# Performance work log

Measured on AMD Instinct MI355X. Metric: run time of the kernel, lower is better.

Reference implementation:

```python
import jax, jax.numpy as jnp
import numpy as np

V, D, H, L, S, B, FF, MAXLEN = 50257, 768, 12, 12, 1024, 4, 3072, 1024
HD = D // H
EPS = 1e-5


def layernorm(x, w, b):
    m = jnp.mean(x, axis=-1, keepdims=True)
    v = jnp.mean(jnp.square(x - m), axis=-1, keepdims=True)
    return (x - m) * jax.lax.rsqrt(v + EPS) * w + b


def setup_inputs() -> dict:
    key = jax.random.key(0)
    ks = jax.random.split(key, 8)
    std = 0.02
    return {
        "tokens": jax.random.randint(ks[0], (B, S), 0, V, dtype=jnp.int32),
        "wte": std * jax.random.normal(ks[1], (V, D), jnp.float32),
        "wpe": std * jax.random.normal(ks[2], (1, MAXLEN, D), jnp.float32),
        "ln1_w": jnp.ones((L, D), jnp.float32),
        "ln1_b": jnp.zeros((L, D), jnp.float32),
        "ln2_w": jnp.ones((L, D), jnp.float32),
        "ln2_b": jnp.zeros((L, D), jnp.float32),
        "W_exp": std * jax.random.normal(ks[3], (L, D, 3 * D), jnp.float32),
        "b_exp": jnp.zeros((L, 3 * D), jnp.float32),
        "W_o": std * jax.random.normal(ks[4], (L, D, D), jnp.float32),
        "b_o": jnp.zeros((L, D), jnp.float32),
        "W_ff1": std * jax.random.normal(ks[5], (L, D, FF), jnp.float32),
        "b_ff1": jnp.zeros((L, FF), jnp.float32),
        "W_ff2": std * jax.random.normal(ks[6], (L, FF, D), jnp.float32),
        "b_ff2": jnp.zeros((L, D), jnp.float32),
    }


def reference(tokens, wte, wpe, ln1_w, ln1_b, ln2_w, ln2_b,
              W_exp, b_exp, W_o, b_o, W_ff1, b_ff1, W_ff2, b_ff2):
    Bc, Sc = tokens.shape
    x = wte[tokens] + wpe[:, :Sc, :]                      # [B,S,D]
    mask = jnp.tril(jnp.ones((Sc, Sc), bool))             # causal (past=None)
    scale = 1.0 / jnp.sqrt(jnp.float32(HD))
    presents = []
    for l in range(L):
        h = layernorm(x, ln1_w[l], ln1_b[l])
        qkv = h @ W_exp[l] + b_exp[l]                     # [B,S,3D]
        q, k, v = jnp.split(qkv, 3, axis=-1)
        q = q.reshape(Bc, Sc, H, HD)
        k = k.reshape(Bc, Sc, H, HD)
        v = v.reshape(Bc, Sc, H, HD)
        presents.append(jnp.stack([k, v]))                # [2,B,S,H,HD]
        score = jnp.einsum('bqhd,bkhd->bhqk', q, k)
        score = jnp.where(mask, score, jnp.float32(-1e20))
        attn = jax.nn.softmax(score * scale, axis=-1)     # mask applied BEFORE scaling, as in source
        a = jnp.einsum('bhqk,bkhd->bqhd', attn, v).reshape(Bc, Sc, D)
        a = a @ W_o[l] + b_o[l]
        add = layernorm(a + x, ln2_w[l], ln2_b[l])        # LN2 on residual sum (GPT2-variant in source)
        ff = jax.nn.gelu(add @ W_ff1[l] + b_ff1[l], approximate=False)
        ff = ff @ W_ff2[l] + b_ff2[l]
        x = ff + add
    return x, jnp.stack(presents)                         # [L,2,B,S,H,HD]
```

## Files before the change

kernel.cpp:

```cpp
#include <hip/hip_runtime.h>
#include <hip/hip_bf16.h>
#include <math.h>

#define Bc 4
#define Sc 1024
#define Dc 768
#define Hc 12
#define Lc 12
#define FFc 3072
#define Mtot (Bc*Sc)

typedef __bf16 bf16x8 __attribute__((ext_vector_type(8)));
typedef float f32x4 __attribute__((ext_vector_type(4)));

__device__ __forceinline__ void gload_lds16(const void* g, void* l) {
    __builtin_amdgcn_global_load_lds((const __attribute__((address_space(1))) void*)g,
                                     (__attribute__((address_space(3))) void*)l, 16, 0, 0);
}

__global__ __launch_bounds__(256) void embed_kernel(const int* __restrict__ tokens,
                                                    const float* __restrict__ wte,
                                                    const float* __restrict__ wpe,
                                                    float* __restrict__ x) {
    int row = blockIdx.x;
    int s = row & (Sc - 1);
    int tok = tokens[row];
    const float* wt = wte + (size_t)tok * Dc;
    const float* wp = wpe + (size_t)s * Dc;
    float* xr = x + (size_t)row * Dc;
#pragma unroll
    for (int k = 0; k < 3; ++k) {
        int d = threadIdx.x + k * 256;
        xr[d] = wt[d] + wp[d];
    }
}

__global__ __launch_bounds__(256) void transpose_kernel(const float* __restrict__ W,
                                                        __bf16* __restrict__ WT,
                                                        int K, int N) {
    __shared__ float t[32][33];
    int l = blockIdx.z;
    const float* Wl = W + (size_t)l * K * N;
    __bf16* WTl = WT + (size_t)l * K * N;
    int n0 = blockIdx.x * 32, k0 = blockIdx.y * 32;
    int tx = threadIdx.x & 31, ty = threadIdx.x >> 5;
#pragma unroll
    for (int i = 0; i < 4; ++i)
        t[ty + 8 * i][tx] = Wl[(size_t)(k0 + ty + 8 * i) * N + n0 + tx];
    __syncthreads();
#pragma unroll
    for (int i = 0; i < 4; ++i)
        WTl[(size_t)(n0 + ty + 8 * i) * K + k0 + tx] = (__bf16)t[tx][ty + 8 * i];
}

template <bool DUAL>
__global__ __launch_bounds__(256) void ln_kernel(const float* __restrict__ x,
                                                 const float* __restrict__ lw,
                                                 const float* __restrict__ lb,
                                                 __bf16* __restrict__ outb,
                                                 float* __restrict__ outf) {
    int row = blockIdx.x;
    const float* xr = x + (size_t)row * Dc;
    int t = threadIdx.x;
    float v0 = xr[t], v1 = xr[t + 256], v2 = xr[t + 512];
    float s1 = v0 + v1 + v2;
    float s2 = v0 * v0 + v1 * v1 + v2 * v2;
    __shared__ float red[8];
#pragma unroll
    for (int o = 32; o; o >>= 1) {
        s1 += __shfl_down(s1, o);
        s2 += __shfl_down(s2, o);
    }
    int wv = t >> 6;
    if ((t & 63) == 0) { red[wv] = s1; red[4 + wv] = s2; }
    __syncthreads();
    float S1 = red[0] + red[1] + red[2] + red[3];
    float S2 = red[4] + red[5] + red[6] + red[7];
    float mean = S1 * (1.0f / Dc);
    float var = S2 * (1.0f / Dc) - mean * mean;
    float rs = rsqrtf(var + 1e-5f);
    size_t ro = (size_t)row * Dc;
    float o0 = (v0 - mean) * rs * lw[t]       + lb[t];
    float o1 = (v1 - mean) * rs * lw[t + 256] + lb[t + 256];
    float o2 = (v2 - mean) * rs * lw[t + 512] + lb[t + 512];
    outb[ro + t]       = (__bf16)o0;
    outb[ro + t + 256] = (__bf16)o1;
    outb[ro + t + 512] = (__bf16)o2;
    if (DUAL) {
        outf[ro + t]       = o0;
        outf[ro + t + 256] = o1;
        outf[ro + t + 512] = o2;
    }
}

template <int BM, int BK, int EPI>
__global__ __launch_bounds__(256) void gemm_bf16(const __bf16* __restrict__ A,
                                                 const __bf16* __restrict__ BT,
                                                 const float* __restrict__ bias,
                                                 const float* __restrict__ addin,
                                                 float* __restrict__ Cf,
                                                 __bf16* __restrict__ Cb,
                                                 float* __restrict__ pres,
                                                 int K, int N) {
    constexpr int HR  = BM / 32;
    constexpr int KS  = BK / 32;
    constexpr int LPR = BK / 8;
    constexpr int SSH = (BK == 32) ? 1 : 0;
    static_assert(BM * BK == 4096, "two staging issues per operand");
    __shared__ __bf16 As[2][BM * BK];
    __shared__ __bf16 Bs[2][BM * BK];
    int tid = threadIdx.x;
    int w = tid >> 6, l = tid & 63;
    int wrow = (w >> 1) * (BM / 2), wcol = (w & 1) * (BM / 2);
    int brow0 = blockIdx.x * BM, bcol0 = blockIdx.y * BM;
    int rsel = l & 15, lg = l >> 4;

    f32x4 acc[HR][HR] = {};

    const __bf16* Abase = A + (size_t)brow0 * K;
    const __bf16* Bbase = BT + (size_t)bcol0 * K;

    auto stage = [&](int buf, int kt) {
#pragma unroll
        for (int i = 0; i < 2; ++i) {
            int cid = i * 256 + w * 64 + l;
            int row = cid / LPR;
            int chunk = (l & (LPR - 1)) ^ ((row >> SSH) & (LPR - 1));
            gload_lds16(Abase + (size_t)row * K + kt + chunk * 8,
                        &As[buf][i * 2048 + w * 512]);
            gload_lds16(Bbase + (size_t)row * K + kt + chunk * 8,
                        &Bs[buf][i * 2048 + w * 512]);
        }
    };

    stage(0, 0);
    __syncthreads();
    int nk = K / BK;
    for (int kt = 0; kt < nk; ++kt) {
        int cur = kt & 1;
        if (kt + 1 < nk) stage(cur ^ 1, (kt + 1) * BK);
        bf16x8 af[KS][HR], bfr[KS][HR];
#pragma unroll
        for (int m = 0; m < HR; ++m) {
            int r = wrow + m * 16 + rsel;
            int sw = (r >> SSH) & (LPR - 1);
#pragma unroll
            for (int s = 0; s < KS; ++s)
                af[s][m] = *(const bf16x8*)(&As[cur][r * BK + ((s * 4 + lg) ^ sw) * 8]);
        }
#pragma unroll
        for (int n = 0; n < HR; ++n) {
            int r = wcol + n * 16 + rsel;
            int sw = (r >> SSH) & (LPR - 1);
#pragma unroll
            for (int s = 0; s < KS; ++s)
                bfr[s][n] = *(const bf16x8*)(&Bs[cur][r * BK + ((s * 4 + lg) ^ sw) * 8]);
        }
#pragma unroll
        for (int s = 0; s < KS; ++s)
#pragma unroll
            for (int m = 0; m < HR; ++m)
#pragma unroll
                for (int n = 0; n < HR; ++n)
                    acc[m][n] = __builtin_amdgcn_mfma_f32_16x16x32_bf16(af[s][m], bfr[s][n], acc[m][n], 0, 0, 0);
        __syncthreads();
    }

    int r4 = lg * 4, cc = rsel;
#pragma unroll
    for (int m = 0; m < HR; ++m)
#pragma unroll
        for (int n = 0; n < HR; ++n) {
            int col = bcol0 + wcol + n * 16 + cc;
            float bv = bias[col];
#pragma unroll
            for (int i = 0; i < 4; ++i) {
                int row = brow0 + wrow + m * 16 + r4 + i;
                float v = acc[m][n][i] + bv;
                if (EPI == 1) {
                    v += addin[(size_t)row * N + col];
                    Cf[(size_t)row * N + col] = v;
                }
                if (EPI == 2) {
                    v = 0.5f * v * (1.0f + erff(v * 0.70710678118654752f));
                    Cb[(size_t)row * N + col] = (__bf16)v;
                }
                if (EPI == 3) {
                    Cb[(size_t)row * N + col] = (__bf16)v;
                    if (col >= 768) {
                        int kv = (col >= 1536) ? 1 : 0;
                        pres[((size_t)kv * Mtot + row) * Dc + (col - 768 - kv * 768)] = v;
                    }
                }
            }
        }
}

__global__ __launch_bounds__(256) void attn_mfma_kernel(const __bf16* __restrict__ qkvb,
                                                        __bf16* __restrict__ aout) {
    __shared__ __bf16 Ks[64 * 72];
    __shared__ __bf16 Vts[64 * 72];
    __shared__ __bf16 Ps[4][16 * 72];
    int bh = blockIdx.x;
    int b = bh / Hc, h = bh % Hc;
    int qt = (Sc / 64 - 1) - blockIdx.y;
    int tid = threadIdx.x;
    int w = tid >> 6, l = tid & 63;
    int lr = l & 15, lg = l >> 4;
    int qb = qt * 64;

    const __bf16* base = qkvb + (size_t)b * Sc * 2304 + h * 64;

    bf16x8 qf[2];
    {
        const __bf16* qrow = base + (size_t)(qb + w * 16 + lr) * 2304 + lg * 8;
        qf[0] = *(const bf16x8*)(qrow);
        qf[1] = *(const bf16x8*)(qrow + 32);
    }

    f32x4 O[4] = {};
    float mrow[4], lrowv[4];
#pragma unroll
    for (int i = 0; i < 4; ++i) { mrow[i] = -1e30f; lrowv[i] = 0.0f; }

    int kj = tid >> 2, kc = tid & 3;
    int vj = tid & 63, vd0 = (tid >> 6) * 8;

    for (int t = 0; t <= qt; ++t) {
        __syncthreads();
#pragma unroll
        for (int it = 0; it < 2; ++it) {
            int c = kc + 4 * it;
            bf16x8 v = *(const bf16x8*)(base + (size_t)(t * 64 + kj) * 2304 + 768 + c * 8);
            *(bf16x8*)(&Ks[kj * 72 + c * 8]) = v;
        }
#pragma unroll
        for (int it = 0; it < 2; ++it) {
            int d0 = vd0 + 32 * it;
            bf16x8 v = *(const bf16x8*)(base + (size_t)(t * 64 + vj) * 2304 + 1536 + d0);
#pragma unroll
            for (int i = 0; i < 8; ++i)
                Vts[(d0 + i) * 72 + vj] = v[i];
        }
        __syncthreads();

        f32x4 sc[4] = {};
#pragma unroll
        for (int s = 0; s < 2; ++s)
#pragma unroll
            for (int n = 0; n < 4; ++n) {
                bf16x8 kf = *(const bf16x8*)(&Ks[(n * 16 + lr) * 72 + s * 32 + lg * 8]);
                sc[n] = __builtin_amdgcn_mfma_f32_16x16x32_bf16(qf[s], kf, sc[n], 0, 0, 0);
            }

        bool diag = (t == qt);
#pragma unroll
        for (int n = 0; n < 4; ++n)
#pragma unroll
            for (int i = 0; i < 4; ++i) {
                float s = sc[n][i] * 0.125f;
                if (diag) {
                    int jg = n * 16 + lr;
                    int qg = w * 16 + lg * 4 + i;
                    if (jg > qg) s = -1e30f;
                }
                sc[n][i] = s;
            }
        float corr[4], psum[4];
#pragma unroll
        for (int i = 0; i < 4; ++i) {
            float mx = fmaxf(fmaxf(sc[0][i], sc[1][i]), fmaxf(sc[2][i], sc[3][i]));
#pragma unroll
            for (int o = 1; o < 16; o <<= 1) mx = fmaxf(mx, __shfl_xor(mx, o));
            float mnew = fmaxf(mrow[i], mx);
            corr[i] = __expf(mrow[i] - mnew);
            mrow[i] = mnew;
            psum[i] = 0.0f;
        }
#pragma unroll
        for (int n = 0; n < 4; ++n)
#pragma unroll
            for (int i = 0; i < 4; ++i) {
                float p = __expf(sc[n][i] - mrow[i]);
                psum[i] += p;
                Ps[w][(lg * 4 + i) * 72 + n * 16 + lr] = (__bf16)p;
            }
#pragma unroll
        for (int i = 0; i < 4; ++i) {
#pragma unroll
            for (int o = 1; o < 16; o <<= 1) psum[i] += __shfl_xor(psum[i], o);
            lrowv[i] = lrowv[i] * corr[i] + psum[i];
        }
#pragma unroll
        for (int n = 0; n < 4; ++n)
#pragma unroll
            for (int i = 0; i < 4; ++i) O[n][i] *= corr[i];
#pragma unroll
        for (int s = 0; s < 2; ++s) {
            bf16x8 pf = *(const bf16x8*)(&Ps[w][lr * 72 + s * 32 + lg * 8]);
#pragma unroll
            for (int n = 0; n < 4; ++n) {
                bf16x8 vf = *(const bf16x8*)(&Vts[(n * 16 + lr) * 72 + s * 32 + lg * 8]);
                O[n] = __builtin_amdgcn_mfma_f32_16x16x32_bf16(pf, vf, O[n], 0, 0, 0);
            }
        }
    }
    __bf16* orow = aout + (size_t)(b * Sc + qb + w * 16 + lg * 4) * Dc + h * 64 + lr;
#pragma unroll
    for (int n = 0; n < 4; ++n)
#pragma unroll
        for (int i = 0; i < 4; ++i)
            orow[(size_t)i * Dc + n * 16] = (__bf16)(O[n][i] / lrowv[i]);
}

__global__ __launch_bounds__(256) void copy_kernel(const float* __restrict__ src,
                                                   float* __restrict__ dst) {
    size_t idx = ((size_t)blockIdx.x * 256 + threadIdx.x) * 4;
    *(float4*)(dst + idx) = *(const float4*)(src + idx);
}

extern "C" void kernel_launch(void* const* d_in, const int* in_sizes, int n_in,
                              void* d_out, int out_size, void* d_ws, size_t ws_size,
                              hipStream_t stream) {
    const int*   tokens = (const int*)d_in[0];
    const float* wte    = (const float*)d_in[1];
    const float* wpe    = (const float*)d_in[2];
    const float* ln1_w  = (const float*)d_in[3];
    const float* ln1_b  = (const float*)d_in[4];
    const float* ln2_w  = (const float*)d_in[5];
    const float* ln2_b  = (const float*)d_in[6];
    const float* W_exp  = (const float*)d_in[7];
    const float* b_exp  = (const float*)d_in[8];
    const float* W_o    = (const float*)d_in[9];
    const float* b_o    = (const float*)d_in[10];
    const float* W_ff1  = (const float*)d_in[11];
    const float* b_ff1  = (const float*)d_in[12];
    const float* W_ff2  = (const float*)d_in[13];
    const float* b_ff2  = (const float*)d_in[14];

    float* out_x    = (float*)d_out;
    float* out_pres = out_x + (size_t)Mtot * Dc;

    float* ws   = (float*)d_ws;
    float* x    = ws;
    float* addf = x + (size_t)Mtot * Dc;
    __bf16* hb   = (__bf16*)(addf + (size_t)Mtot * Dc);
    __bf16* addb = hb + (size_t)Mtot * Dc;
    __bf16* qkvb = addb + (size_t)Mtot * Dc;
    __bf16* ff1b = qkvb + (size_t)Mtot * 3 * Dc;
    __bf16* wt_exp = ff1b + (size_t)Mtot * FFc;
    __bf16* wt_o   = wt_exp + (size_t)Lc * 2304 * 768;
    __bf16* wt_ff1 = wt_o   + (size_t)Lc * 768 * 768;
    __bf16* wt_ff2 = wt_ff1 + (size_t)Lc * 3072 * 768;

    embed_kernel<<<Mtot, 256, 0, stream>>>(tokens, wte, wpe, x);

    transpose_kernel<<<dim3(2304 / 32, 768 / 32, Lc), 256, 0, stream>>>(W_exp, wt_exp, 768, 2304);
    transpose_kernel<<<dim3(768 / 32, 768 / 32, Lc), 256, 0, stream>>>(W_o, wt_o, 768, 768);
    transpose_kernel<<<dim3(3072 / 32, 768 / 32, Lc), 256, 0, stream>>>(W_ff1, wt_ff1, 768, 3072);
    transpose_kernel<<<dim3(768 / 32, 3072 / 32, Lc), 256, 0, stream>>>(W_ff2, wt_ff2, 3072, 768);

    for (int lidx = 0; lidx < Lc; ++lidx) {
        ln_kernel<false><<<Mtot, 256, 0, stream>>>(
            x, ln1_w + lidx * Dc, ln1_b + lidx * Dc, hb, nullptr);
        gemm_bf16<128, 32, 3><<<dim3(Mtot / 128, 2304 / 128), 256, 0, stream>>>(
            hb, wt_exp + (size_t)lidx * 2304 * 768, b_exp + (size_t)lidx * 3 * Dc,
            nullptr, nullptr, qkvb, out_pres + (size_t)lidx * 2 * Mtot * Dc, 768, 2304);
        attn_mfma_kernel<<<dim3(Bc * Hc, Sc / 64), 256, 0, stream>>>(qkvb, hb);
        gemm_bf16<64, 64, 1><<<dim3(Mtot / 64, 768 / 64), 256, 0, stream>>>(
            hb, wt_o + (size_t)lidx * 768 * 768, b_o + (size_t)lidx * Dc,
            x, x, nullptr, nullptr, 768, 768);
        ln_kernel<true><<<Mtot, 256, 0, stream>>>(
            x, ln2_w + lidx * Dc, ln2_b + lidx * Dc, addb, addf);
        gemm_bf16<128, 32, 2><<<dim3(Mtot / 128, FFc / 128), 256, 0, stream>>>(
            addb, wt_ff1 + (size_t)lidx * 3072 * 768, b_ff1 + (size_t)lidx * FFc,
            nullptr, nullptr, ff1b, nullptr, 768, FFc);
        gemm_bf16<64, 64, 1><<<dim3(Mtot / 64, 768 / 64), 256, 0, stream>>>(
            ff1b, wt_ff2 + (size_t)lidx * 768 * 3072, b_ff2 + (size_t)lidx * Dc,
            addf, x, nullptr, nullptr, 3072, 768);
    }

    copy_kernel<<<((size_t)Mtot * Dc) / (256 * 4), 256, 0, stream>>>(x, out_x);
}
```

Measured before the change: 2.278 ms.

## Use rectangular GEMM tiles, per-layer fused weight transpose, write final output directly

```diff
diff --git a/kernel.cpp b/kernel.cpp
--- a/kernel.cpp
+++ b/kernel.cpp
@@ -35,22 +35,28 @@
     }
 }
 
-__global__ __launch_bounds__(256) void transpose_kernel(const float* __restrict__ W,
-                                                        __bf16* __restrict__ WT,
-                                                        int K, int N) {
-    __shared__ float t[32][33];
-    int l = blockIdx.z;
-    const float* Wl = W + (size_t)l * K * N;
-    __bf16* WTl = WT + (size_t)l * K * N;
-    int n0 = blockIdx.x * 32, k0 = blockIdx.y * 32;
+__global__ __launch_bounds__(256) void transpose_all_kernel(
+        const float* __restrict__ We, const float* __restrict__ Wo,
+        const float* __restrict__ Wf1, const float* __restrict__ Wf2,
+        __bf16* __restrict__ Te, __bf16* __restrict__ To,
+        __bf16* __restrict__ Tf1, __bf16* __restrict__ Tf2) {
+    __shared__ float tl[32][33];
+    int bid = blockIdx.x;
+    const float* W; __bf16* T; int K, N, t;
+    if (bid < 1728)      { W = We;  T = Te;  K = 768;  N = 2304; t = bid; }
+    else if (bid < 2304) { W = Wo;  T = To;  K = 768;  N = 768;  t = bid - 1728; }
+    else if (bid < 4608) { W = Wf1; T = Tf1; K = 768;  N = 3072; t = bid - 2304; }
+    else                 { W = Wf2; T = Tf2; K = 3072; N = 768;  t = bid - 4608; }
+    int nx = N >> 5;
+    int n0 = (t % nx) * 32, k0 = (t / nx) * 32;
     int tx = threadIdx.x & 31, ty = threadIdx.x >> 5;
 #pragma unroll
     for (int i = 0; i < 4; ++i)
-        t[ty + 8 * i][tx] = Wl[(size_t)(k0 + ty + 8 * i) * N + n0 + tx];
+        tl[ty + 8 * i][tx] = W[(size_t)(k0 + ty + 8 * i) * N + n0 + tx];
     __syncthreads();
 #pragma unroll
     for (int i = 0; i < 4; ++i)
-        WTl[(size_t)(n0 + ty + 8 * i) * K + k0 + tx] = (__bf16)t[tx][ty + 8 * i];
+        T[(size_t)(n0 + ty + 8 * i) * K + k0 + tx] = (__bf16)tl[tx][ty + 8 * i];
 }
 
 template <bool DUAL>
@@ -93,7 +99,7 @@
     }
 }
 
-template <int BM, int BK, int EPI>
+template <int BMr, int BNc, int BK, int EPI>
 __global__ __launch_bounds__(256) void gemm_bf16(const __bf16* __restrict__ A,
                                                  const __bf16* __restrict__ BT,
                                                  const float* __restrict__ bias,
@@ -102,34 +108,42 @@
                                                  __bf16* __restrict__ Cb,
                                                  float* __restrict__ pres,
                                                  int K, int N) {
-    constexpr int HR  = BM / 32;
+    constexpr int HRm = BMr / 32, HRn = BNc / 32;
     constexpr int KS  = BK / 32;
     constexpr int LPR = BK / 8;
     constexpr int SSH = (BK == 32) ? 1 : 0;
-    static_assert(BM * BK == 4096, "two staging issues per operand");
-    __shared__ __bf16 As[2][BM * BK];
-    __shared__ __bf16 Bs[2][BM * BK];
+    constexpr int IA  = BMr * BK / 2048;
+    constexpr int IB  = BNc * BK / 2048;
+    static_assert(IA >= 1 && IB >= 1, "tile too small");
+    __shared__ __bf16 As[2][BMr * BK];
+    __shared__ __bf16 Bs[2][BNc * BK];
     int tid = threadIdx.x;
     int w = tid >> 6, l = tid & 63;
-    int wrow = (w >> 1) * (BM / 2), wcol = (w & 1) * (BM / 2);
-    int brow0 = blockIdx.x * BM, bcol0 = blockIdx.y * BM;
+    int wrow = (w >> 1) * (BMr / 2), wcol = (w & 1) * (BNc / 2);
+    int brow0 = blockIdx.x * BMr, bcol0 = blockIdx.y * BNc;
     int rsel = l & 15, lg = l >> 4;
 
-    f32x4 acc[HR][HR] = {};
+    f32x4 acc[HRm][HRn] = {};
 
     const __bf16* Abase = A + (size_t)brow0 * K;
     const __bf16* Bbase = BT + (size_t)bcol0 * K;
 
     auto stage = [&](int buf, int kt) {
 #pragma unroll
-        for (int i = 0; i < 2; ++i) {
-            int cid = i * 256 + w * 64 + l;
-            int row = cid / LPR;
-            int chunk = (l & (LPR - 1)) ^ ((row >> SSH) & (LPR - 1));
+        for (int i = 0; i < IA; ++i) {
+            int cid = i * 256 + tid;
+            int row = cid / LPR, slot = cid % LPR;
+            int chunk = slot ^ ((row >> SSH) & (LPR - 1));
             gload_lds16(Abase + (size_t)row * K + kt + chunk * 8,
-                        &As[buf][i * 2048 + w * 512]);
+                        &As[buf][(i * 256 + w * 64) * 8]);
+        }
+#pragma unroll
+        for (int i = 0; i < IB; ++i) {
+            int cid = i * 256 + tid;
+            int row = cid / LPR, slot = cid % LPR;
+            int chunk = slot ^ ((row >> SSH) & (LPR - 1));
             gload_lds16(Bbase + (size_t)row * K + kt + chunk * 8,
-                        &Bs[buf][i * 2048 + w * 512]);
+                        &Bs[buf][(i * 256 + w * 64) * 8]);
         }
     };
 
@@ -139,9 +153,9 @@
     for (int kt = 0; kt < nk; ++kt) {
         int cur = kt & 1;
         if (kt + 1 < nk) stage(cur ^ 1, (kt + 1) * BK);
-        bf16x8 af[KS][HR], bfr[KS][HR];
-#pragma unroll
-        for (int m = 0; m < HR; ++m) {
+        bf16x8 af[KS][HRm], bfr[KS][HRn];
+#pragma unroll
+        for (int m = 0; m < HRm; ++m) {
             int r = wrow + m * 16 + rsel;
             int sw = (r >> SSH) & (LPR - 1);
 #pragma unroll
@@ -149,7 +163,7 @@
                 af[s][m] = *(const bf16x8*)(&As[cur][r * BK + ((s * 4 + lg) ^ sw) * 8]);
         }
 #pragma unroll
-        for (int n = 0; n < HR; ++n) {
+        for (int n = 0; n < HRn; ++n) {
             int r = wcol + n * 16 + rsel;
             int sw = (r >> SSH) & (LPR - 1);
 #pragma unroll
@@ -159,18 +173,18 @@
 #pragma unroll
         for (int s = 0; s < KS; ++s)
 #pragma unroll
-            for (int m = 0; m < HR; ++m)
-#pragma unroll
-                for (int n = 0; n < HR; ++n)
+            for (int m = 0; m < HRm; ++m)
+#pragma unroll
+                for (int n = 0; n < HRn; ++n)
                     acc[m][n] = __builtin_amdgcn_mfma_f32_16x16x32_bf16(af[s][m], bfr[s][n], acc[m][n], 0, 0, 0);
         __syncthreads();
     }
 
     int r4 = lg * 4, cc = rsel;
 #pragma unroll
-    for (int m = 0; m < HR; ++m)
-#pragma unroll
-        for (int n = 0; n < HR; ++n) {
+    for (int m = 0; m < HRm; ++m)
+#pragma unroll
+        for (int n = 0; n < HRn; ++n) {
             int col = bcol0 + wcol + n * 16 + cc;
             float bv = bias[col];
 #pragma unroll
@@ -313,12 +327,6 @@
             orow[(size_t)i * Dc + n * 16] = (__bf16)(O[n][i] / lrowv[i]);
 }
 
-__global__ __launch_bounds__(256) void copy_kernel(const float* __restrict__ src,
-                                                   float* __restrict__ dst) {
-    size_t idx = ((size_t)blockIdx.x * 256 + threadIdx.x) * 4;
-    *(float4*)(dst + idx) = *(const float4*)(src + idx);
-}
-
 extern "C" void kernel_launch(void* const* d_in, const int* in_sizes, int n_in,
                               void* d_out, int out_size, void* d_ws, size_t ws_size,
                               hipStream_t stream) {
@@ -349,36 +357,35 @@
     __bf16* qkvb = addb + (size_t)Mtot * Dc;
     __bf16* ff1b = qkvb + (size_t)Mtot * 3 * Dc;
     __bf16* wt_exp = ff1b + (size_t)Mtot * FFc;
-    __bf16* wt_o   = wt_exp + (size_t)Lc * 2304 * 768;
-    __bf16* wt_ff1 = wt_o   + (size_t)Lc * 768 * 768;
-    __bf16* wt_ff2 = wt_ff1 + (size_t)Lc * 3072 * 768;
+    __bf16* wt_o   = wt_exp + (size_t)2304 * 768;
+    __bf16* wt_ff1 = wt_o   + (size_t)768 * 768;
+    __bf16* wt_ff2 = wt_ff1 + (size_t)3072 * 768;
 
     embed_kernel<<<Mtot, 256, 0, stream>>>(tokens, wte, wpe, x);
 
-    transpose_kernel<<<dim3(2304 / 32, 768 / 32, Lc), 256, 0, stream>>>(W_exp, wt_exp, 768, 2304);
-    transpose_kernel<<<dim3(768 / 32, 768 / 32, Lc), 256, 0, stream>>>(W_o, wt_o, 768, 768);
-    transpose_kernel<<<dim3(3072 / 32, 768 / 32, Lc), 256, 0, stream>>>(W_ff1, wt_ff1, 768, 3072);
-    transpose_kernel<<<dim3(768 / 32, 3072 / 32, Lc), 256, 0, stream>>>(W_ff2, wt_ff2, 3072, 768);
-
     for (int lidx = 0; lidx < Lc; ++lidx) {
+        transpose_all_kernel<<<6912, 256, 0, stream>>>(
+            W_exp + (size_t)lidx * 768 * 2304, W_o + (size_t)lidx * 768 * 768,
+            W_ff1 + (size_t)lidx * 768 * 3072, W_ff2 + (size_t)lidx * 3072 * 768,
+            wt_exp, wt_o, wt_ff1, wt_ff2);
+
         ln_kernel<false><<<Mtot, 256, 0, stream>>>(
             x, ln1_w + lidx * Dc, ln1_b + lidx * Dc, hb, nullptr);
-        gemm_bf16<128, 32, 3><<<dim3(Mtot / 128, 2304 / 128), 256, 0, stream>>>(
-            hb, wt_exp + (size_t)lidx * 2304 * 768, b_exp + (size_t)lidx * 3 * Dc,
+        gemm_bf16<128, 128, 32, 3><<<dim3(Mtot / 128, 2304 / 128), 256, 0, stream>>>(
+            hb, wt_exp, b_exp + (size_t)lidx * 3 * Dc,
             nullptr, nullptr, qkvb, out_pres + (size_t)lidx * 2 * Mtot * Dc, 768, 2304);
         attn_mfma_kernel<<<dim3(Bc * Hc, Sc / 64), 256, 0, stream>>>(qkvb, hb);
-        gemm_bf16<64, 64, 1><<<dim3(Mtot / 64, 768 / 64), 256, 0, stream>>>(
-            hb, wt_o + (size_t)lidx * 768 * 768, b_o + (size_t)lidx * Dc,
+        gemm_bf16<128, 64, 64, 1><<<dim3(Mtot / 128, 768 / 64), 256, 0, stream>>>(
+            hb, wt_o, b_o + (size_t)lidx * Dc,
             x, x, nullptr, nullptr, 768, 768);
         ln_kernel<true><<<Mtot, 256, 0, stream>>>(
             x, ln2_w + lidx * Dc, ln2_b + lidx * Dc, addb, addf);
-        gemm_bf16<128, 32, 2><<<dim3(Mtot / 128, FFc / 128), 256, 0, stream>>>(
-            addb, wt_ff1 + (size_t)lidx * 3072 * 768, b_ff1 + (size_t)lidx * FFc,
+        gemm_bf16<128, 128, 32, 2><<<dim3(Mtot / 128, FFc / 128), 256, 0, stream>>>(
+            addb, wt_ff1, b_ff1 + (size_t)lidx * FFc,
             nullptr, nullptr, ff1b, nullptr, 768, FFc);
-        gemm_bf16<64, 64, 1><<<dim3(Mtot / 64, 768 / 64), 256, 0, stream>>>(
-            ff1b, wt_ff2 + (size_t)lidx * 768 * 3072, b_ff2 + (size_t)lidx * Dc,
-            addf, x, nullptr, nullptr, 3072, 768);
-    }
-
-    copy_kernel<<<((size_t)Mtot * Dc) / (256 * 4), 256, 0, stream>>>(x, out_x);
-}
+        float* ff2dst = (lidx == Lc - 1) ? out_x : x;
+        gemm_bf16<128, 64, 64, 1><<<dim3(Mtot / 128, 768 / 64), 256, 0, stream>>>(
+            ff1b, wt_ff2, b_ff2 + (size_t)lidx * Dc,
+            addf, ff2dst, nullptr, nullptr, 3072, 768);
+    }
+}
```

Result: faster. 2.114 ms (-7.2%).
